# Optimization experiments

Hardware: AMD Instinct MI355X
Metric: run time of the kernel (lower is better)

## Reference

```python
import jax, jax.numpy as jnp
import numpy as np

C_S, C_P, FEAT_DIM, NUM_BINS = 256, 128, 64, 22
TOTAL_EDGE_FEATS = FEAT_DIM * 3 + NUM_BINS * 2  # 236
MAX_LEN = 2056


def get_index_embedding(indices, embed_size, max_len=MAX_LEN):
    # indices: [..., ] float; returns [..., embed_size]
    K = jnp.arange(embed_size // 2, dtype=jnp.float32)
    ang = indices[..., None] * jnp.pi / (max_len ** (2.0 * K / embed_size))
    return jnp.concatenate([jnp.sin(ang), jnp.cos(ang)], axis=-1)


def calc_distogram(pos, min_bin, max_bin, num_bins):
    # pos: [B, N, 3] -> one-hot distogram [B, N, N, num_bins]
    d = jnp.linalg.norm(pos[:, :, None, :] - pos[:, None, :, :], axis=-1)[..., None]
    lower = jnp.linspace(min_bin, max_bin, num_bins)
    upper = jnp.concatenate([lower[1:], jnp.array([1e8], dtype=jnp.float32)])
    return ((d > lower) & (d < upper)).astype(pos.dtype)


def layer_norm(x, gamma, beta, eps=1e-5):
    mu = jnp.mean(x, axis=-1, keepdims=True)
    var = jnp.mean((x - mu) ** 2, axis=-1, keepdims=True)
    return (x - mu) * jax.lax.rsqrt(var + eps) * gamma + beta


def setup_inputs() -> dict:
    key = jax.random.key(0)
    ks = jax.random.split(key, 12)
    B, N = 2, 512
    def lin(k, fan_in, shape):
        bound = 1.0 / np.sqrt(fan_in)
        return jax.random.uniform(k, shape, jnp.float32, -bound, bound)
    return {
        "s": jax.random.normal(ks[0], (B, N, C_S), jnp.float32),
        "t": jax.random.normal(ks[1], (B, N, 3), jnp.float32),
        "sc_t": jax.random.normal(ks[2], (B, N, 3), jnp.float32),
        "p_mask": jnp.ones((B, N, N), jnp.float32),
        "W_sp": lin(ks[3], C_S, (FEAT_DIM, C_S)),
        "b_sp": lin(ks[4], C_S, (FEAT_DIM,)),
        "W_rp": lin(ks[5], FEAT_DIM, (FEAT_DIM, FEAT_DIM)),
        "b_rp": lin(ks[5], FEAT_DIM, (FEAT_DIM,)),
        "W1": lin(ks[6], TOTAL_EDGE_FEATS, (C_P, TOTAL_EDGE_FEATS)),
        "b1": lin(ks[7], TOTAL_EDGE_FEATS, (C_P,)),
        "W2": lin(ks[8], C_P, (C_P, C_P)),
        "b2": lin(ks[9], C_P, (C_P,)),
        "W3": lin(ks[10], C_P, (C_P, C_P)),
        "b3": lin(ks[11], C_P, (C_P,)),
        "ln_g": jnp.ones((C_P,), jnp.float32),
        "ln_b": jnp.zeros((C_P,), jnp.float32),
    }


def reference(s, t, sc_t, p_mask, W_sp, b_sp, W_rp, b_rp, W1, b1, W2, b2, W3, b3, ln_g, ln_b):
    B, N, _ = s.shape
    # node embed then all-pairs broadcast-concat: [B,N,N,2*feat_dim]
    p_i = s @ W_sp.T + b_sp  # [B,N,feat_dim]
    cross = jnp.concatenate([
        jnp.broadcast_to(p_i[:, :, None, :], (B, N, N, FEAT_DIM)),
        jnp.broadcast_to(p_i[:, None, :, :], (B, N, N, FEAT_DIM)),
    ], axis=-1)
    # relative position embedding (res_idx=None -> arange)
    pos = jnp.broadcast_to(jnp.arange(N, dtype=jnp.float32)[None, :], (B, N))
    rel_pos = pos[:, :, None] - pos[:, None, :]
    pos_emb = get_index_embedding(rel_pos, FEAT_DIM)  # [B,N,N,feat_dim]
    relpos_feats = pos_emb @ W_rp.T + b_rp
    dist_feats = calc_distogram(t, 1e-3, 20.0, NUM_BINS)
    sc_feats = calc_distogram(sc_t, 1e-3, 20.0, NUM_BINS)
    all_edge = jnp.concatenate([cross, relpos_feats, dist_feats, sc_feats], axis=-1)
    h = jax.nn.relu(all_edge @ W1.T + b1)
    h = jax.nn.relu(h @ W2.T + b2)
    h = h @ W3.T + b3
    h = layer_norm(h, ln_g, ln_b)
    return h * p_mask[..., None]
```

## Files before the change

### kernel.cpp

```cpp
#include <hip/hip_runtime.h>

#define NN 512

typedef __attribute__((ext_vector_type(8))) short bf16x8;
typedef __attribute__((ext_vector_type(4))) float f32x4;

__device__ __forceinline__ unsigned short f2bf(float x) {
    union { float f; unsigned u; } c; c.f = x;
    unsigned u = c.u + 0x7fffu + ((c.u >> 16) & 1u);
    return (unsigned short)(u >> 16);
}

__device__ __forceinline__ float blo(unsigned u) {
    union { unsigned x; float f; } c; c.x = u << 16; return c.f;
}
__device__ __forceinline__ float bhi(unsigned u) {
    union { unsigned x; float f; } c; c.x = u & 0xffff0000u; return c.f;
}

__device__ __forceinline__ unsigned pk2(unsigned a, unsigned b, unsigned c,
                                        unsigned d, unsigned e) {
    float lo = blo(a) + blo(b) + blo(c) + blo(d) + blo(e);
    float hi = bhi(a) + bhi(b) + bhi(c) + bhi(d) + bhi(e);
    lo = fmaxf(lo, 0.0f);
    hi = fmaxf(hi, 0.0f);
    return (unsigned)f2bf(lo) | ((unsigned)f2bf(hi) << 16);
}

__device__ __forceinline__ int find_bin(float d) {
    int bin = 22;
    #pragma unroll
    for (int k = 0; k < 22; ++k) {
        float lo = (float)(1e-3 + k * ((20.0 - 1e-3) / 21.0));
        float hi = (k < 21) ? (float)(1e-3 + (k + 1) * ((20.0 - 1e-3) / 21.0)) : 1e8f;
        if (d > lo && d < hi) bin = k;
    }
    return bin;
}

__global__ __launch_bounds__(128) void k_prep(
        const float* __restrict__ s, const float* __restrict__ t,
        const float* __restrict__ sct,
        const float* __restrict__ Wsp, const float* __restrict__ bsp,
        const float* __restrict__ Wrp, const float* __restrict__ brp,
        const float* __restrict__ W1, const float* __restrict__ b1,
        const float* __restrict__ W2, const float* __restrict__ W3,
        float* __restrict__ p_i, unsigned short* __restrict__ relTb,
        unsigned short* __restrict__ WdTb, unsigned short* __restrict__ WscTb,
        unsigned short* __restrict__ w2a, unsigned short* __restrict__ w3a,
        unsigned short* __restrict__ binT)
{
    __shared__ float sh[2][256];
    const int blk = blockIdx.x, tid = threadIdx.x;

    if (blk < 23) {
        const int bin = blk, c = tid;
        WdTb[bin * 128 + c]  = (bin < 22) ? f2bf(W1[c * 236 + 192 + bin]) : (unsigned short)0;
        WscTb[bin * 128 + c] = (bin < 22) ? f2bf(W1[c * 236 + 214 + bin]) : (unsigned short)0;
    } else if (blk < 55) {
        const int seg = blk - 23;
        const int isW3 = seg >> 4;
        const int idx = (seg & 15) * 128 + tid;
        const int lane = idx & 63, ks = (idx >> 6) & 3, ct = idx >> 8;
        const float* W = isW3 ? W3 : W2;
        unsigned short* dst = isW3 ? w3a : w2a;
        const float* wp = W + (ct * 16 + (lane & 15)) * 128 + ks * 32 + (lane >> 4) * 8;
        unsigned r0 = (unsigned)f2bf(wp[0]) | ((unsigned)f2bf(wp[1]) << 16);
        unsigned r1 = (unsigned)f2bf(wp[2]) | ((unsigned)f2bf(wp[3]) << 16);
        unsigned r2 = (unsigned)f2bf(wp[4]) | ((unsigned)f2bf(wp[5]) << 16);
        unsigned r3 = (unsigned)f2bf(wp[6]) | ((unsigned)f2bf(wp[7]) << 16);
        uint4 v = { r0, r1, r2, r3 };
        *(uint4*)(dst + idx * 8) = v;
    } else if (blk < 1078) {
        const int row = blk - 55;
        const float d = (float)(row - 511);
        if (tid < 32) {
            float f = powf(2056.0f, (float)tid * (1.0f / 32.0f));
            float ang = d * 3.14159265358979323846f / f;
            sh[0][tid] = sinf(ang);
            sh[0][tid + 32] = cosf(ang);
        }
        __syncthreads();
        if (tid < 64) {
            const float* wr = Wrp + tid * 64;
            float a = brp[tid];
            #pragma unroll
            for (int k = 0; k < 64; ++k) a += sh[0][k] * wr[k];
            sh[1][tid] = a;
        }
        __syncthreads();
        const float* w = W1 + tid * 236 + 128;
        float a = b1[tid];
        #pragma unroll
        for (int k = 0; k < 64; ++k) a += sh[1][k] * w[k];
        relTb[row * 128 + tid] = f2bf(a);
    } else if (blk < 1590) {
        const int half = tid >> 6, ch = tid & 63;
        const int row = (blk - 1078) * 2 + half;
        *(float4*)&sh[half][ch * 4] = *(const float4*)&s[row * 256 + ch * 4];
        __syncthreads();
        const float* w = Wsp + ch * 256;
        float acc = bsp[ch];
        #pragma unroll 8
        for (int k = 0; k < 256; k += 4)
            acc += sh[half][k]*w[k] + sh[half][k+1]*w[k+1] + sh[half][k+2]*w[k+2] + sh[half][k+3]*w[k+3];
        p_i[row * 64 + ch] = acc;
    } else {
        const int pair = (blk - 1590) * 128 + tid;
        const int bi = pair >> 9, j = pair & (NN - 1);
        const int rj = (bi & ~(NN - 1)) + j;
        float ax = t[bi*3+0] - t[rj*3+0];
        float ay = t[bi*3+1] - t[rj*3+1];
        float az = t[bi*3+2] - t[rj*3+2];
        int bD = find_bin(sqrtf(ax*ax + ay*ay + az*az));
        float sx = sct[bi*3+0] - sct[rj*3+0];
        float sy = sct[bi*3+1] - sct[rj*3+1];
        float sz = sct[bi*3+2] - sct[rj*3+2];
        int bS = find_bin(sqrtf(sx*sx + sy*sy + sz*sz));
        binT[pair] = (unsigned short)(bD | (bS << 5));
    }
}

__global__ __launch_bounds__(128) void k_ql(const float* __restrict__ p_i,
        const float* __restrict__ W1,
        unsigned short* __restrict__ qLb, unsigned short* __restrict__ qRb)
{
    __shared__ float pr[64];
    const int row = blockIdx.x, tid = threadIdx.x;
    if (tid < 16) *(float4*)&pr[tid * 4] = *(const float4*)&p_i[row * 64 + tid * 4];
    __syncthreads();
    const float* w = W1 + tid * 236;
    float aL = 0.f, aR = 0.f;
    #pragma unroll
    for (int k = 0; k < 64; ++k) { aL += pr[k] * w[k]; aR += pr[k] * w[64 + k]; }
    qLb[row * 128 + tid] = f2bf(aL);
    qRb[row * 128 + tid] = f2bf(aR);
}

#define H1_OFF  0
#define H2_OFF  16384
#define WD_OFF  32768
#define WSC_OFF 39024
#define LNP_OFF 45280
#define SMEM_SZ 50400

__global__ __launch_bounds__(512, 4) void k_main(
    const float* __restrict__ pmask,
    const unsigned short* __restrict__ qLb, const unsigned short* __restrict__ qRb,
    const unsigned short* __restrict__ relTb, const unsigned short* __restrict__ WdTb,
    const unsigned short* __restrict__ WscTb, const unsigned short* __restrict__ binT,
    const unsigned short* __restrict__ w2a, const unsigned short* __restrict__ w3a,
    const float* __restrict__ b2, const float* __restrict__ b3,
    const float* __restrict__ lng, const float* __restrict__ lnb,
    float* __restrict__ out)
{
    __shared__ __align__(16) char smem[SMEM_SZ];

    const int tid  = threadIdx.x;
    const int l    = tid & 63;
    const int w    = tid >> 6;
    const int jloc = l & 15;
    const int gq   = l >> 4;

    const int blk   = blockIdx.x;
    const int bi    = blk >> 3;
    const int i     = bi & (NN - 1);
    const int bbase = bi & ~(NN - 1);
    const int j0    = (blk & 7) * 64;

    bf16x8 w2r[4], w3r[4];
    #pragma unroll
    for (int ks = 0; ks < 4; ++ks) {
        w2r[ks] = *(const bf16x8*)(w2a + (w * 256 + ks * 64 + l) * 8);
        w3r[ks] = *(const bf16x8*)(w3a + (w * 256 + ks * 64 + l) * 8);
    }
    const int cch = w * 16 + gq * 4;
    const float4 b2f = *(const float4*)(b2 + cch);
    const float4 b3f = *(const float4*)(b3 + cch);
    const float4 g4  = *(const float4*)(lng + cch);
    const float4 be4 = *(const float4*)(lnb + cch);
    float maskv[4];
    #pragma unroll
    for (int tt = 0; tt < 4; ++tt)
        maskv[tt] = pmask[(size_t)bi * NN + j0 + tt * 16 + jloc];

    #pragma unroll
    for (int it = 0; it < 2; ++it) {
        int idx = it * 512 + tid;
        if (idx < 736) {
            int tb = idx >= 368;
            int k = idx - (tb ? 368 : 0);
            int row = k >> 4, off = k & 15;
            const unsigned short* src = (tb ? WscTb : WdTb) + row * 128 + off * 8;
            *(uint4*)(smem + (tb ? WSC_OFF : WD_OFF) + row * 272 + off * 16) =
                *(const uint4*)src;
        }
    }
    __syncthreads();

    {
        const int r = tid >> 3, q = tid & 7;
        const unsigned bv = binT[bi * NN + j0 + r];
        const int bD = bv & 31, bS = (int)(bv >> 5);
        const unsigned short* qLp = qLb + (size_t)bi * 128;
        const unsigned short* qRp = qRb + (size_t)(bbase + j0 + r) * 128;
        const unsigned short* rTp = relTb + (size_t)(i - (j0 + r) + NN - 1) * 128;
        const int hswz = (r & 7) << 4;
        #pragma unroll
        for (int u = 0; u < 2; ++u) {
            const int c0 = q * 16 + u * 8;
            uint4 A = *(const uint4*)(qLp + c0);
            uint4 B = *(const uint4*)(qRp + c0);
            uint4 C = *(const uint4*)(rTp + c0);
            uint4 D = *(const uint4*)(smem + WD_OFF + bD * 272 + c0 * 2);
            uint4 E = *(const uint4*)(smem + WSC_OFF + bS * 272 + c0 * 2);
            uint4 P;
            P.x = pk2(A.x, B.x, C.x, D.x, E.x);
            P.y = pk2(A.y, B.y, C.y, D.y, E.y);
            P.z = pk2(A.z, B.z, C.z, D.z, E.z);
            P.w = pk2(A.w, B.w, C.w, D.w, E.w);
            *(uint4*)(smem + H1_OFF + ((r * 256 + c0 * 2) ^ hswz)) = P;
        }
    }
    __syncthreads();

    const int rswz = (jloc & 7) << 4;

    #pragma unroll
    for (int tt = 0; tt < 4; ++tt) {
        const int rowb = (tt * 16 + jloc) * 256;
        f32x4 a2 = {0.f, 0.f, 0.f, 0.f};
        #pragma unroll
        for (int ks = 0; ks < 4; ++ks) {
            bf16x8 bfr = *(bf16x8*)(smem + H1_OFF + ((rowb + ks * 64 + gq * 16) ^ rswz));
            a2 = __builtin_amdgcn_mfma_f32_16x16x32_bf16(w2r[ks], bfr, a2, 0, 0, 0);
        }
        float y0 = fmaxf(a2[0] + b2f.x, 0.0f);
        float y1 = fmaxf(a2[1] + b2f.y, 0.0f);
        float y2 = fmaxf(a2[2] + b2f.z, 0.0f);
        float y3 = fmaxf(a2[3] + b2f.w, 0.0f);
        uint2 pk;
        pk.x = (unsigned)f2bf(y0) | ((unsigned)f2bf(y1) << 16);
        pk.y = (unsigned)f2bf(y2) | ((unsigned)f2bf(y3) << 16);
        *(uint2*)(smem + H2_OFF + ((rowb + cch * 2) ^ rswz)) = pk;
    }
    __syncthreads();

    f32x4 acc3[4];
    float* lnp = (float*)(smem + LNP_OFF);
    #pragma unroll
    for (int tt = 0; tt < 4; ++tt) {
        const int rowb = (tt * 16 + jloc) * 256;
        f32x4 a3 = {0.f, 0.f, 0.f, 0.f};
        #pragma unroll
        for (int ks = 0; ks < 4; ++ks) {
            bf16x8 bfr = *(bf16x8*)(smem + H2_OFF + ((rowb + ks * 64 + gq * 16) ^ rswz));
            a3 = __builtin_amdgcn_mfma_f32_16x16x32_bf16(w3r[ks], bfr, a3, 0, 0, 0);
        }
        a3[0] += b3f.x; a3[1] += b3f.y; a3[2] += b3f.z; a3[3] += b3f.w;
        acc3[tt] = a3;
        float s1 = a3[0] + a3[1] + a3[2] + a3[3];
        float s2 = a3[0]*a3[0] + a3[1]*a3[1] + a3[2]*a3[2] + a3[3]*a3[3];
        s1 += __shfl_xor(s1, 16); s2 += __shfl_xor(s2, 16);
        s1 += __shfl_xor(s1, 32); s2 += __shfl_xor(s2, 32);
        if (l < 16) {
            float2 p2 = make_float2(s1, s2);
            *(float2*)(lnp + (tt * 16 + jloc) * 20 + w * 2) = p2;
        }
    }
    __syncthreads();

    #pragma unroll
    for (int tt = 0; tt < 4; ++tt) {
        const int row = tt * 16 + jloc;
        float s1 = 0.f, s2 = 0.f;
        #pragma unroll
        for (int pp = 0; pp < 4; ++pp) {
            float4 v = *(float4*)(lnp + row * 20 + pp * 4);
            s1 += v.x + v.z; s2 += v.y + v.w;
        }
        const float mean = s1 * (1.0f / 128.0f);
        const float var  = s2 * (1.0f / 128.0f) - mean * mean;
        const float rstd = rsqrtf(var + 1e-5f);
        const float mk = maskv[tt];
        f32x4 a3 = acc3[tt];
        float4 o;
        o.x = ((a3[0] - mean) * rstd * g4.x + be4.x) * mk;
        o.y = ((a3[1] - mean) * rstd * g4.y + be4.y) * mk;
        o.z = ((a3[2] - mean) * rstd * g4.z + be4.z) * mk;
        o.w = ((a3[3] - mean) * rstd * g4.w + be4.w) * mk;
        *(float4*)(out + ((size_t)(bi * NN + j0 + row)) * 128 + cch) = o;
    }
}

extern "C" void kernel_launch(void* const* d_in, const int* in_sizes, int n_in,
                              void* d_out, int out_size, void* d_ws, size_t ws_size,
                              hipStream_t stream)
{
    const float* s   = (const float*)d_in[0];
    const float* t   = (const float*)d_in[1];
    const float* sct = (const float*)d_in[2];
    const float* pm  = (const float*)d_in[3];
    const float* Wsp = (const float*)d_in[4];
    const float* bsp = (const float*)d_in[5];
    const float* Wrp = (const float*)d_in[6];
    const float* brp = (const float*)d_in[7];
    const float* W1  = (const float*)d_in[8];
    const float* b1  = (const float*)d_in[9];
    const float* W2  = (const float*)d_in[10];
    const float* b2  = (const float*)d_in[11];
    const float* W3  = (const float*)d_in[12];
    const float* b3  = (const float*)d_in[13];
    const float* lng = (const float*)d_in[14];
    const float* lnb = (const float*)d_in[15];

    float* ws = (float*)d_ws;
    float*          p_i   = ws;
    unsigned short* qLb   = (unsigned short*)(ws + 65536);
    unsigned short* qRb   = (unsigned short*)(ws + 131072);
    unsigned short* relTb = (unsigned short*)(ws + 196608);
    unsigned short* WdTb  = (unsigned short*)(ws + 262144);
    unsigned short* WscTb = (unsigned short*)(ws + 263616);
    unsigned short* w2a   = (unsigned short*)(ws + 265088);
    unsigned short* w3a   = (unsigned short*)(ws + 273280);
    unsigned short* binT  = (unsigned short*)(ws + 281472);

    k_prep<<<5686, 128, 0, stream>>>(s, t, sct, Wsp, bsp, Wrp, brp, W1, b1, W2, W3,
                                     p_i, relTb, WdTb, WscTb, w2a, w3a, binT);
    k_ql<<<1024, 128, 0, stream>>>(p_i, W1, qLb, qRb);
    k_main<<<8192, 512, 0, stream>>>(pm, qLb, qRb, relTb, WdTb, WscTb, binT,
                                     w2a, w3a, b2, b3, lng, lnb, (float*)d_out);
}
```

Baseline: 147.5 us.

## Read distogram weights from global memory and stage output through LDS for coalesced stores

The distogram and self-conditioning weight tables are no longer copied into shared memory at the start of each block. They are read directly from global memory, which are small, cache-resident tables, and this removes one barrier and some LDS footprint. The final layer-norm output is written into a swizzled shared-memory tile and then written out with fully contiguous nontemporal 16-byte stores, where before each lane wrote scattered float4s. The trade is an extra barrier and LDS round trip for the output, plus more global or L2 gathers for the weight rows.

```diff
diff --git a/kernel.cpp b/kernel.cpp
--- a/kernel.cpp
+++ b/kernel.cpp
@@ -139,10 +139,8 @@
 
 #define H1_OFF  0
 #define H2_OFF  16384
-#define WD_OFF  32768
-#define WSC_OFF 39024
-#define LNP_OFF 45280
-#define SMEM_SZ 50400
+#define LNP_OFF 32768
+#define SMEM_SZ 37888
 
 __global__ __launch_bounds__(512, 4) void k_main(
     const float* __restrict__ pmask,
@@ -184,20 +182,6 @@
     for (int tt = 0; tt < 4; ++tt)
         maskv[tt] = pmask[(size_t)bi * NN + j0 + tt * 16 + jloc];
 
-    #pragma unroll
-    for (int it = 0; it < 2; ++it) {
-        int idx = it * 512 + tid;
-        if (idx < 736) {
-            int tb = idx >= 368;
-            int k = idx - (tb ? 368 : 0);
-            int row = k >> 4, off = k & 15;
-            const unsigned short* src = (tb ? WscTb : WdTb) + row * 128 + off * 8;
-            *(uint4*)(smem + (tb ? WSC_OFF : WD_OFF) + row * 272 + off * 16) =
-                *(const uint4*)src;
-        }
-    }
-    __syncthreads();
-
     {
         const int r = tid >> 3, q = tid & 7;
         const unsigned bv = binT[bi * NN + j0 + r];
@@ -205,6 +189,8 @@
         const unsigned short* qLp = qLb + (size_t)bi * 128;
         const unsigned short* qRp = qRb + (size_t)(bbase + j0 + r) * 128;
         const unsigned short* rTp = relTb + (size_t)(i - (j0 + r) + NN - 1) * 128;
+        const unsigned short* dTp = WdTb + bD * 128;
+        const unsigned short* sTp = WscTb + bS * 128;
         const int hswz = (r & 7) << 4;
         #pragma unroll
         for (int u = 0; u < 2; ++u) {
@@ -212,8 +198,8 @@
             uint4 A = *(const uint4*)(qLp + c0);
             uint4 B = *(const uint4*)(qRp + c0);
             uint4 C = *(const uint4*)(rTp + c0);
-            uint4 D = *(const uint4*)(smem + WD_OFF + bD * 272 + c0 * 2);
-            uint4 E = *(const uint4*)(smem + WSC_OFF + bS * 272 + c0 * 2);
+            uint4 D = *(const uint4*)(dTp + c0);
+            uint4 E = *(const uint4*)(sTp + c0);
             uint4 P;
             P.x = pk2(A.x, B.x, C.x, D.x, E.x);
             P.y = pk2(A.y, B.y, C.y, D.y, E.y);
@@ -284,12 +270,25 @@
         const float rstd = rsqrtf(var + 1e-5f);
         const float mk = maskv[tt];
         f32x4 a3 = acc3[tt];
-        float4 o;
-        o.x = ((a3[0] - mean) * rstd * g4.x + be4.x) * mk;
-        o.y = ((a3[1] - mean) * rstd * g4.y + be4.y) * mk;
-        o.z = ((a3[2] - mean) * rstd * g4.z + be4.z) * mk;
-        o.w = ((a3[3] - mean) * rstd * g4.w + be4.w) * mk;
-        *(float4*)(out + ((size_t)(bi * NN + j0 + row)) * 128 + cch) = o;
+        f32x4 o;
+        o[0] = ((a3[0] - mean) * rstd * g4.x + be4.x) * mk;
+        o[1] = ((a3[1] - mean) * rstd * g4.y + be4.y) * mk;
+        o[2] = ((a3[2] - mean) * rstd * g4.z + be4.z) * mk;
+        o[3] = ((a3[3] - mean) * rstd * g4.w + be4.w) * mk;
+        const int slot = (w * 4 + gq) ^ (row & 31);
+        *(f32x4*)(smem + row * 512 + slot * 16) = o;
+    }
+    __syncthreads();
+
+    float* ob = out + ((size_t)(bi * NN + j0)) * 128;
+    #pragma unroll
+    for (int it = 0; it < 4; ++it) {
+        const int boff = it * 8192 + tid * 16;
+        const int row  = boff >> 9;
+        const int slot = (boff >> 4) & 31;
+        const int sslt = slot ^ (row & 31);
+        f32x4 v = *(f32x4*)(smem + row * 512 + sslt * 16);
+        __builtin_nontemporal_store(v, (f32x4*)(ob + (boff >> 2)));
     }
 }
 
```

Result: faster. 128.4 us (-12.9%).
